# Kernel tuning notes

Hardware: AMD Instinct MI355X
Metric: run time of the kernel (lower is better)

The kernel has to match this reference:

```python
import jax, jax.numpy as jnp
import numpy as np

NEG_INF = -1e9  # additive mask value (every row attends to itself, so softmax is safe)


def setup_inputs() -> dict:
    D, H, N = 256, 8, 4096
    key = jax.random.key(0)
    ks = jax.random.split(key, 7)
    slots = jax.random.normal(ks[0], (1, N, D), dtype=jnp.float32)
    batch_idx = jnp.sort(jax.random.randint(ks[1], (N,), 0, 16)).astype(jnp.int32)
    s_in = 1.0 / np.sqrt(D)
    w_in = jax.random.uniform(ks[2], (3 * D, D), jnp.float32, -s_in, s_in)
    b_in = jnp.zeros((3 * D,), jnp.float32)
    w_out = jax.random.uniform(ks[3], (D, D), jnp.float32, -s_in, s_in)
    b_out = jnp.zeros((D,), jnp.float32)
    ln_gamma = jnp.ones((D,), jnp.float32)
    ln_beta = jnp.zeros((D,), jnp.float32)
    return {"slots": slots, "batch_idx": batch_idx, "w_in": w_in, "b_in": b_in,
            "w_out": w_out, "b_out": b_out, "ln_gamma": ln_gamma, "ln_beta": ln_beta}


def _mha_block_diag(x, batch_idx, w_in, b_in, w_out, b_out, num_heads):
    # x: [N, D]
    N, D = x.shape
    hd = D // num_heads
    qkv = x @ w_in.T + b_in                      # [N, 3D]
    q, k, v = jnp.split(qkv, 3, axis=-1)
    q = q.reshape(N, num_heads, hd).transpose(1, 0, 2)   # [H, N, hd]
    k = k.reshape(N, num_heads, hd).transpose(1, 0, 2)
    v = v.reshape(N, num_heads, hd).transpose(1, 0, 2)
    scale = 1.0 / np.sqrt(hd)
    scores = jnp.einsum('hnd,hmd->hnm', q, k) * scale    # [H, N, N]
    mask = batch_idx[:, None] != batch_idx[None, :]      # True = blocked
    scores = jnp.where(mask[None], NEG_INF, scores)
    attn = jax.nn.softmax(scores, axis=-1)
    out = jnp.einsum('hnm,hmd->hnd', attn, v)            # [H, N, hd]
    out = out.transpose(1, 0, 2).reshape(N, D)
    return out @ w_out.T + b_out


def _layer_norm(x, gamma, beta, eps=1e-5):
    mu = jnp.mean(x, axis=-1, keepdims=True)
    var = jnp.mean(jnp.square(x - mu), axis=-1, keepdims=True)
    return (x - mu) * jax.lax.rsqrt(var + eps) * gamma + beta


def reference(slots, batch_idx, w_in, b_in, w_out, b_out, ln_gamma, ln_beta):
    # slots: [1, N, D]; dropout prob is 0.0 (eval-mode reference)
    x = slots[0]
    delta = _mha_block_diag(x, batch_idx, w_in, b_in, w_out, b_out, num_heads=8)
    out = _layer_norm(x + delta, ln_gamma, ln_beta)
    return out[None]
```

## Files before the change

### kernel.cpp

```cpp
#include <hip/hip_runtime.h>
#include <hip/hip_bf16.h>

#define NROWS 4096
#define DMODEL 256
#define NHEADS 8
#define HD 32

typedef __attribute__((ext_vector_type(8))) short short8;
typedef __attribute__((ext_vector_type(4))) float f32x4;

__global__ __launch_bounds__(256) void cast_bf16_kernel(
    const float* __restrict__ src, __hip_bfloat16* __restrict__ dst, int n) {
  const int i = (blockIdx.x * 256 + threadIdx.x) * 4;
  if (i >= n) return;
  const float4 v = *(const float4*)(src + i);
  __hip_bfloat162 lo, hi;
  lo.x = __float2bfloat16(v.x); lo.y = __float2bfloat16(v.y);
  hi.x = __float2bfloat16(v.z); hi.y = __float2bfloat16(v.w);
  *(__hip_bfloat162*)(dst + i) = lo;
  *(__hip_bfloat162*)(dst + i + 2) = hi;
}

__device__ __forceinline__ void load_lds16(const void* g, void* l) {
  __builtin_amdgcn_global_load_lds(
      (const __attribute__((address_space(1))) unsigned int*)g,
      (__attribute__((address_space(3))) unsigned int*)l, 16, 0, 0);
}

template<bool SCATTER>
__global__ __launch_bounds__(256) void gemm_mfma(
    const __hip_bfloat16* __restrict__ A, const __hip_bfloat16* __restrict__ B,
    const float* __restrict__ bias, float* __restrict__ C,
    __hip_bfloat16* __restrict__ Qo, __hip_bfloat16* __restrict__ Ko,
    __hip_bfloat16* __restrict__ Vo,
    int Nd, int K) {
  __shared__ __hip_bfloat16 As[128][32];
  __shared__ __hip_bfloat16 Bs[128][32];
  const int tid  = threadIdx.x;
  const int w    = tid >> 6;
  const int lane = tid & 63;
  const int lo16 = lane & 15;
  const int quad = lane >> 4;
  const int bm = blockIdx.y * 128;
  const int bn = blockIdx.x * 128;
  const int wm = (w & 1) * 64;
  const int wn = (w >> 1) * 64;

  f32x4 acc[4][4] = {};

  const int fbase = w * 2048;

  for (int k0 = 0; k0 < K; k0 += 32) {
    #pragma unroll
    for (int inst = 0; inst < 2; inst++) {
      const int f   = fbase + inst * 1024 + lane * 16;
      const int row = f >> 6;
      const int kb  = (f & 63) >> 1;
      load_lds16(A + (size_t)(bm + row) * K + k0 + kb,
                 (char*)&As[0][0] + fbase + inst * 1024);
      load_lds16(B + (size_t)(bn + row) * K + k0 + kb,
                 (char*)&Bs[0][0] + fbase + inst * 1024);
    }
    __syncthreads();
    short8 af[4], bf[4];
    #pragma unroll
    for (int i = 0; i < 4; i++) {
      af[i] = *(const short8*)&As[wm + i * 16 + lo16][quad * 8];
      bf[i] = *(const short8*)&Bs[wn + i * 16 + lo16][quad * 8];
    }
    #pragma unroll
    for (int mi = 0; mi < 4; mi++)
      #pragma unroll
      for (int ni = 0; ni < 4; ni++)
        acc[mi][ni] = __builtin_amdgcn_mfma_f32_16x16x32_bf16(
            af[mi], bf[ni], acc[mi][ni], 0, 0, 0);
    __syncthreads();
  }

  #pragma unroll
  for (int mi = 0; mi < 4; mi++) {
    const int rbase = bm + wm + mi * 16 + quad * 4;
    #pragma unroll
    for (int ni = 0; ni < 4; ni++) {
      const int col = bn + wn + ni * 16 + lo16;
      const float bv = bias[col];
      #pragma unroll
      for (int r = 0; r < 4; r++) {
        const int n = rbase + r;
        const float v = acc[mi][ni][r] + bv;
        if (SCATTER) {
          const int sel = col >> 8;
          const int h = (col & 255) >> 5;
          const int d = col & 31;
          const __hip_bfloat16 bv16 = __float2bfloat16(v);
          if (sel == 0)      Qo[((size_t)h * NROWS + n) * HD + d] = bv16;
          else if (sel == 1) Ko[((size_t)h * NROWS + n) * HD + d] = bv16;
          else               Vo[((size_t)h * HD + d) * NROWS + n] = bv16;
        } else {
          C[(size_t)n * Nd + col] = v;
        }
      }
    }
  }
}

__global__ void seg_kernel(const int* __restrict__ bidx, int* __restrict__ segs) {
  const int r = blockIdx.x * 256 + threadIdx.x;
  if (r >= NROWS) return;
  const int b = bidx[r];
  if (r == 0 || bidx[r - 1] != b) segs[b] = r;
  if (r == NROWS - 1 || bidx[r + 1] != b) segs[16 + b] = r + 1;
}

__global__ __launch_bounds__(256) void attn_mfma(
    const __hip_bfloat16* __restrict__ Qb,
    const __hip_bfloat16* __restrict__ Kb,
    const __hip_bfloat16* __restrict__ Vt,
    const int* __restrict__ bidx,
    const int* __restrict__ segs,
    __hip_bfloat16* __restrict__ out)
{
  __shared__ __align__(16) __hip_bfloat16 Plds_all[4][16][40];
  const int wv   = threadIdx.x >> 6;
  const int lane = threadIdx.x & 63;
  const int wid  = blockIdx.x * 4 + wv;
  const int qt   = wid >> 3;
  const int h    = wid & 7;
  const int r0   = qt * 16;
  const int lo16 = lane & 15;
  const int quad = lane >> 4;
  __hip_bfloat16 (*Plds)[40] = Plds_all[wv];

  int rb[4];
  #pragma unroll
  for (int r = 0; r < 4; r++) rb[r] = bidx[r0 + quad * 4 + r];

  const int kstart = segs[bidx[r0]] & ~31;
  const int kend   = segs[16 + bidx[r0 + 15]];

  const short8 qf = *(const short8*)(Qb + ((size_t)h * NROWS + r0 + lo16) * HD + quad * 8);

  f32x4 o0 = {0.f, 0.f, 0.f, 0.f}, o1 = {0.f, 0.f, 0.f, 0.f};
  float m[4], l[4];
  #pragma unroll
  for (int r = 0; r < 4; r++) { m[r] = -1e30f; l[r] = 0.0f; }

  const float scale = 0.17677669529663687f;

  for (int c0 = kstart; c0 < kend; c0 += 32) {
    const int col0 = c0 + lo16;
    const int col1 = col0 + 16;
    const int colc0 = min(col0, NROWS - 1);
    const int colc1 = min(col1, NROWS - 1);
    const short8 kf0 = *(const short8*)(Kb + ((size_t)h * NROWS + colc0) * HD + quad * 8);
    const short8 kf1 = *(const short8*)(Kb + ((size_t)h * NROWS + colc1) * HD + quad * 8);
    const int vc = min(c0 + quad * 8, NROWS - 8);
    const short8 vf0 = *(const short8*)(Vt + ((size_t)h * HD + lo16) * NROWS + vc);
    const short8 vf1 = *(const short8*)(Vt + ((size_t)h * HD + 16 + lo16) * NROWS + vc);
    const int cb0 = bidx[colc0];
    const int cb1 = bidx[colc1];

    f32x4 z = {0.f, 0.f, 0.f, 0.f};
    f32x4 s0 = __builtin_amdgcn_mfma_f32_16x16x32_bf16(qf, kf0, z, 0, 0, 0);
    f32x4 s1 = __builtin_amdgcn_mfma_f32_16x16x32_bf16(qf, kf1, z, 0, 0, 0);

    float p0[4], p1[4];
    #pragma unroll
    for (int r = 0; r < 4; r++) {
      const bool ok0 = (col0 < NROWS) && (cb0 == rb[r]);
      const bool ok1 = (col1 < NROWS) && (cb1 == rb[r]);
      const float sc0 = ok0 ? s0[r] * scale : -1e30f;
      const float sc1 = ok1 ? s1[r] * scale : -1e30f;
      float mx = fmaxf(sc0, sc1);
      mx = fmaxf(mx, __shfl_xor(mx, 1));
      mx = fmaxf(mx, __shfl_xor(mx, 2));
      mx = fmaxf(mx, __shfl_xor(mx, 4));
      mx = fmaxf(mx, __shfl_xor(mx, 8));
      const float nm = fmaxf(m[r], mx);
      const float alpha = __expf(m[r] - nm);
      p0[r] = ok0 ? __expf(sc0 - nm) : 0.0f;
      p1[r] = ok1 ? __expf(sc1 - nm) : 0.0f;
      float ps = p0[r] + p1[r];
      ps += __shfl_xor(ps, 1);
      ps += __shfl_xor(ps, 2);
      ps += __shfl_xor(ps, 4);
      ps += __shfl_xor(ps, 8);
      l[r] = l[r] * alpha + ps;
      m[r] = nm;
      o0[r] *= alpha;
      o1[r] *= alpha;
    }

    #pragma unroll
    for (int r = 0; r < 4; r++) {
      Plds[quad * 4 + r][lo16]      = __float2bfloat16(p0[r]);
      Plds[quad * 4 + r][lo16 + 16] = __float2bfloat16(p1[r]);
    }
    const short8 pf = *(const short8*)&Plds[lo16][quad * 8];

    o0 = __builtin_amdgcn_mfma_f32_16x16x32_bf16(pf, vf0, o0, 0, 0, 0);
    o1 = __builtin_amdgcn_mfma_f32_16x16x32_bf16(pf, vf1, o1, 0, 0, 0);
  }

  #pragma unroll
  for (int r = 0; r < 4; r++) {
    const float inv = 1.0f / l[r];
    const int row = r0 + quad * 4 + r;
    out[(size_t)row * DMODEL + h * HD + lo16]      = __float2bfloat16(o0[r] * inv);
    out[(size_t)row * DMODEL + h * HD + 16 + lo16] = __float2bfloat16(o1[r] * inv);
  }
}

__global__ __launch_bounds__(256) void ln_kernel(
    const float* __restrict__ x, const float* __restrict__ delta,
    const float* __restrict__ gamma, const float* __restrict__ beta,
    float* __restrict__ out) {
  const int n = blockIdx.x;
  const int t = threadIdx.x;
  __shared__ float red[8];
  const float v = x[(size_t)n * DMODEL + t] + delta[(size_t)n * DMODEL + t];
  float s = v;
  #pragma unroll
  for (int off = 32; off; off >>= 1) s += __shfl_xor(s, off);
  const int w = t >> 6;
  if ((t & 63) == 0) red[w] = s;
  __syncthreads();
  const float mean = (red[0] + red[1] + red[2] + red[3]) * (1.0f / DMODEL);
  const float d0 = v - mean;
  float s2 = d0 * d0;
  #pragma unroll
  for (int off = 32; off; off >>= 1) s2 += __shfl_xor(s2, off);
  if ((t & 63) == 0) red[4 + w] = s2;
  __syncthreads();
  const float var = (red[4] + red[5] + red[6] + red[7]) * (1.0f / DMODEL);
  out[(size_t)n * DMODEL + t] = d0 * rsqrtf(var + 1e-5f) * gamma[t] + beta[t];
}

extern "C" void kernel_launch(void* const* d_in, const int* in_sizes, int n_in,
                              void* d_out, int out_size, void* d_ws, size_t ws_size,
                              hipStream_t stream) {
  const float* slots  = (const float*)d_in[0];
  const int*   bidx   = (const int*)  d_in[1];
  const float* w_in   = (const float*)d_in[2];
  const float* b_in   = (const float*)d_in[3];
  const float* w_out  = (const float*)d_in[4];
  const float* b_out  = (const float*)d_in[5];
  const float* ln_g   = (const float*)d_in[6];
  const float* ln_b   = (const float*)d_in[7];
  float* out = (float*)d_out;

  char* ws = (char*)d_ws;
  __hip_bfloat16* Abf   = (__hip_bfloat16*)(ws);
  __hip_bfloat16* Qb    = (__hip_bfloat16*)(ws + (2u  << 20));
  __hip_bfloat16* Kb    = (__hip_bfloat16*)(ws + (4u  << 20));
  __hip_bfloat16* Vt    = (__hip_bfloat16*)(ws + (6u  << 20));
  __hip_bfloat16* attnb = (__hip_bfloat16*)(ws + (8u  << 20));
  float*          proj  = (float*)         (ws + (10u << 20));
  __hip_bfloat16* Winb  = (__hip_bfloat16*)(ws + (14u << 20));
  __hip_bfloat16* Woutb = (__hip_bfloat16*)(ws + (14u << 20) + (512u << 10));
  int*            segs  = (int*)           (ws + (15u << 20));

  cast_bf16_kernel<<<1024, 256, 0, stream>>>(slots, Abf, NROWS * DMODEL);
  cast_bf16_kernel<<<192, 256, 0, stream>>>(w_in, Winb, 768 * DMODEL);
  cast_bf16_kernel<<<64, 256, 0, stream>>>(w_out, Woutb, DMODEL * DMODEL);
  seg_kernel<<<NROWS / 256, 256, 0, stream>>>(bidx, segs);

  {
    dim3 grid(768 / 128, NROWS / 128);
    gemm_mfma<true><<<grid, 256, 0, stream>>>(Abf, Winb, b_in, nullptr,
                                              Qb, Kb, Vt, 768, DMODEL);
  }
  attn_mfma<<<(NROWS / 16) * NHEADS / 4, 256, 0, stream>>>(Qb, Kb, Vt, bidx,
                                                           segs, attnb);
  {
    dim3 grid(DMODEL / 128, NROWS / 128);
    gemm_mfma<false><<<grid, 256, 0, stream>>>(attnb, Woutb, b_out, proj,
                                               nullptr, nullptr, nullptr,
                                               DMODEL, DMODEL);
  }
  ln_kernel<<<NROWS, 256, 0, stream>>>(slots, proj, ln_g, ln_b, out);
}
```

Measured before the change: 131.4 us.

## Fuse prep kernels and widen attention key tile to 128 columns

Merges the three bf16 cast launches and the segment-boundary kernel into one prep kernel, removing three launches. The attention loop now handles 128 key columns per iteration instead of 32: it loads 8 K fragments and 4 V pairs up front, issues 8 score MFMAs, and masks by per-row segment ranges rather than per-column batch-index loads. This amortises the online-softmax reductions and rescaling over more columns and drops the bidx gathers. The cost is higher register pressure (launch bounds set to 2 blocks), a larger P staging buffer in LDS, and wasted work on partially masked 128-wide tiles at segment edges.

```diff
diff --git a/kernel.cpp b/kernel.cpp
--- a/kernel.cpp
+++ b/kernel.cpp
@@ -9,10 +9,25 @@
 typedef __attribute__((ext_vector_type(8))) short short8;
 typedef __attribute__((ext_vector_type(4))) float f32x4;
 
-__global__ __launch_bounds__(256) void cast_bf16_kernel(
-    const float* __restrict__ src, __hip_bfloat16* __restrict__ dst, int n) {
-  const int i = (blockIdx.x * 256 + threadIdx.x) * 4;
-  if (i >= n) return;
+__global__ __launch_bounds__(256) void prep_kernel(
+    const float* __restrict__ slots, const float* __restrict__ w_in,
+    const float* __restrict__ w_out, const int* __restrict__ bidx,
+    __hip_bfloat16* __restrict__ Abf, __hip_bfloat16* __restrict__ Winb,
+    __hip_bfloat16* __restrict__ Woutb, int* __restrict__ segs) {
+  const int bid = blockIdx.x;
+  const float* src;
+  __hip_bfloat16* dst;
+  int i;
+  if (bid < 1024)      { src = slots; dst = Abf;   i = (bid * 256 + (int)threadIdx.x) * 4; }
+  else if (bid < 1216) { src = w_in;  dst = Winb;  i = ((bid - 1024) * 256 + (int)threadIdx.x) * 4; }
+  else if (bid < 1280) { src = w_out; dst = Woutb; i = ((bid - 1216) * 256 + (int)threadIdx.x) * 4; }
+  else {
+    const int r = (bid - 1280) * 256 + threadIdx.x;
+    const int b = bidx[r];
+    if (r == 0 || bidx[r - 1] != b) segs[b] = r;
+    if (r == NROWS - 1 || bidx[r + 1] != b) segs[16 + b] = r + 1;
+    return;
+  }
   const float4 v = *(const float4*)(src + i);
   __hip_bfloat162 lo, hi;
   lo.x = __float2bfloat16(v.x); lo.y = __float2bfloat16(v.y);
@@ -47,7 +62,6 @@
   const int wn = (w >> 1) * 64;
 
   f32x4 acc[4][4] = {};
-
   const int fbase = w * 2048;
 
   for (int k0 = 0; k0 < K; k0 += 32) {
@@ -104,15 +118,7 @@
   }
 }
 
-__global__ void seg_kernel(const int* __restrict__ bidx, int* __restrict__ segs) {
-  const int r = blockIdx.x * 256 + threadIdx.x;
-  if (r >= NROWS) return;
-  const int b = bidx[r];
-  if (r == 0 || bidx[r - 1] != b) segs[b] = r;
-  if (r == NROWS - 1 || bidx[r + 1] != b) segs[16 + b] = r + 1;
-}
-
-__global__ __launch_bounds__(256) void attn_mfma(
+__global__ __launch_bounds__(256, 2) void attn_mfma(
     const __hip_bfloat16* __restrict__ Qb,
     const __hip_bfloat16* __restrict__ Kb,
     const __hip_bfloat16* __restrict__ Vt,
@@ -120,7 +126,7 @@
     const int* __restrict__ segs,
     __hip_bfloat16* __restrict__ out)
 {
-  __shared__ __align__(16) __hip_bfloat16 Plds_all[4][16][40];
+  __shared__ __align__(16) __hip_bfloat16 Plds_all[4][16][136];
   const int wv   = threadIdx.x >> 6;
   const int lane = threadIdx.x & 63;
   const int wid  = blockIdx.x * 4 + wv;
@@ -129,11 +135,15 @@
   const int r0   = qt * 16;
   const int lo16 = lane & 15;
   const int quad = lane >> 4;
-  __hip_bfloat16 (*Plds)[40] = Plds_all[wv];
-
-  int rb[4];
-  #pragma unroll
-  for (int r = 0; r < 4; r++) rb[r] = bidx[r0 + quad * 4 + r];
+  __hip_bfloat16 (*Plds)[136] = Plds_all[wv];
+
+  int st[4], en[4];
+  #pragma unroll
+  for (int r = 0; r < 4; r++) {
+    const int b = bidx[r0 + quad * 4 + r];
+    st[r] = segs[b];
+    en[r] = segs[16 + b];
+  }
 
   const int kstart = segs[bidx[r0]] & ~31;
   const int kend   = segs[16 + bidx[r0 + 15]];
@@ -147,40 +157,51 @@
 
   const float scale = 0.17677669529663687f;
 
-  for (int c0 = kstart; c0 < kend; c0 += 32) {
-    const int col0 = c0 + lo16;
-    const int col1 = col0 + 16;
-    const int colc0 = min(col0, NROWS - 1);
-    const int colc1 = min(col1, NROWS - 1);
-    const short8 kf0 = *(const short8*)(Kb + ((size_t)h * NROWS + colc0) * HD + quad * 8);
-    const short8 kf1 = *(const short8*)(Kb + ((size_t)h * NROWS + colc1) * HD + quad * 8);
-    const int vc = min(c0 + quad * 8, NROWS - 8);
-    const short8 vf0 = *(const short8*)(Vt + ((size_t)h * HD + lo16) * NROWS + vc);
-    const short8 vf1 = *(const short8*)(Vt + ((size_t)h * HD + 16 + lo16) * NROWS + vc);
-    const int cb0 = bidx[colc0];
-    const int cb1 = bidx[colc1];
-
-    f32x4 z = {0.f, 0.f, 0.f, 0.f};
-    f32x4 s0 = __builtin_amdgcn_mfma_f32_16x16x32_bf16(qf, kf0, z, 0, 0, 0);
-    f32x4 s1 = __builtin_amdgcn_mfma_f32_16x16x32_bf16(qf, kf1, z, 0, 0, 0);
-
-    float p0[4], p1[4];
+  for (int c0 = kstart; c0 < kend; c0 += 128) {
+    short8 kf[8];
+    #pragma unroll
+    for (int j = 0; j < 8; j++) {
+      const int cc = min(c0 + j * 16 + lo16, NROWS - 1);
+      kf[j] = *(const short8*)(Kb + ((size_t)h * NROWS + cc) * HD + quad * 8);
+    }
+    short8 vf[8];
+    #pragma unroll
+    for (int t = 0; t < 4; t++) {
+      const int vc = min(c0 + t * 32 + quad * 8, NROWS - 8);
+      vf[2 * t]     = *(const short8*)(Vt + ((size_t)h * HD + lo16) * NROWS + vc);
+      vf[2 * t + 1] = *(const short8*)(Vt + ((size_t)h * HD + 16 + lo16) * NROWS + vc);
+    }
+    f32x4 s[8];
+    const f32x4 z = {0.f, 0.f, 0.f, 0.f};
+    #pragma unroll
+    for (int j = 0; j < 8; j++)
+      s[j] = __builtin_amdgcn_mfma_f32_16x16x32_bf16(qf, kf[j], z, 0, 0, 0);
+
     #pragma unroll
     for (int r = 0; r < 4; r++) {
-      const bool ok0 = (col0 < NROWS) && (cb0 == rb[r]);
-      const bool ok1 = (col1 < NROWS) && (cb1 == rb[r]);
-      const float sc0 = ok0 ? s0[r] * scale : -1e30f;
-      const float sc1 = ok1 ? s1[r] * scale : -1e30f;
-      float mx = fmaxf(sc0, sc1);
+      float sc[8];
+      #pragma unroll
+      for (int j = 0; j < 8; j++) {
+        const int col = c0 + j * 16 + lo16;
+        const bool ok = (col >= st[r]) & (col < en[r]);
+        sc[j] = ok ? s[j][r] * scale : -1e30f;
+      }
+      float mx = sc[0];
+      #pragma unroll
+      for (int j = 1; j < 8; j++) mx = fmaxf(mx, sc[j]);
       mx = fmaxf(mx, __shfl_xor(mx, 1));
       mx = fmaxf(mx, __shfl_xor(mx, 2));
       mx = fmaxf(mx, __shfl_xor(mx, 4));
       mx = fmaxf(mx, __shfl_xor(mx, 8));
       const float nm = fmaxf(m[r], mx);
       const float alpha = __expf(m[r] - nm);
-      p0[r] = ok0 ? __expf(sc0 - nm) : 0.0f;
-      p1[r] = ok1 ? __expf(sc1 - nm) : 0.0f;
-      float ps = p0[r] + p1[r];
+      float ps = 0.0f;
+      #pragma unroll
+      for (int j = 0; j < 8; j++) {
+        const float p = (sc[j] > -5e29f) ? __expf(sc[j] - nm) : 0.0f;
+        ps += p;
+        Plds[quad * 4 + r][lo16 + j * 16] = __float2bfloat16(p);
+      }
       ps += __shfl_xor(ps, 1);
       ps += __shfl_xor(ps, 2);
       ps += __shfl_xor(ps, 4);
@@ -192,14 +213,11 @@
     }
 
     #pragma unroll
-    for (int r = 0; r < 4; r++) {
-      Plds[quad * 4 + r][lo16]      = __float2bfloat16(p0[r]);
-      Plds[quad * 4 + r][lo16 + 16] = __float2bfloat16(p1[r]);
-    }
-    const short8 pf = *(const short8*)&Plds[lo16][quad * 8];
-
-    o0 = __builtin_amdgcn_mfma_f32_16x16x32_bf16(pf, vf0, o0, 0, 0, 0);
-    o1 = __builtin_amdgcn_mfma_f32_16x16x32_bf16(pf, vf1, o1, 0, 0, 0);
+    for (int t = 0; t < 4; t++) {
+      const short8 pf = *(const short8*)&Plds[lo16][t * 32 + quad * 8];
+      o0 = __builtin_amdgcn_mfma_f32_16x16x32_bf16(pf, vf[2 * t],     o0, 0, 0, 0);
+      o1 = __builtin_amdgcn_mfma_f32_16x16x32_bf16(pf, vf[2 * t + 1], o1, 0, 0, 0);
+    }
   }
 
   #pragma unroll
@@ -260,11 +278,8 @@
   __hip_bfloat16* Woutb = (__hip_bfloat16*)(ws + (14u << 20) + (512u << 10));
   int*            segs  = (int*)           (ws + (15u << 20));
 
-  cast_bf16_kernel<<<1024, 256, 0, stream>>>(slots, Abf, NROWS * DMODEL);
-  cast_bf16_kernel<<<192, 256, 0, stream>>>(w_in, Winb, 768 * DMODEL);
-  cast_bf16_kernel<<<64, 256, 0, stream>>>(w_out, Woutb, DMODEL * DMODEL);
-  seg_kernel<<<NROWS / 256, 256, 0, stream>>>(bidx, segs);
-
+  prep_kernel<<<1296, 256, 0, stream>>>(slots, w_in, w_out, bidx,
+                                        Abf, Winb, Woutb, segs);
   {
     dim3 grid(768 / 128, NROWS / 128);
     gemm_mfma<true><<<grid, 256, 0, stream>>>(Abf, Winb, b_in, nullptr,
```

Measured after the change: 120.8 us. -8.1%, faster.
